# Kernel tuning notes

Hardware: AMD Instinct MI355X
Metric: run time of the kernel (lower is better)

The kernel has to match this reference:

```python
import jax, jax.numpy as jnp
import numpy as np


def setup_inputs() -> dict:
    key = jax.random.key(0)
    ks = jax.random.split(key, 6)
    B, C_in, C_out, H, W = 4, 256, 128, 64, 64
    return {
        "p": jax.random.normal(ks[0], (B, C_in, H, W), dtype=jnp.float32),
        "b": jax.random.normal(ks[1], (B, C_in, H, W), dtype=jnp.float32),
        "Wq": jax.random.normal(ks[2], (C_out, C_in), dtype=jnp.float32) * 0.05,
        "bq": jax.random.normal(ks[3], (C_out,), dtype=jnp.float32) * 0.05,
        "Wk": jax.random.normal(ks[4], (C_out, C_in), dtype=jnp.float32) * 0.05,
        "bk": jax.random.normal(ks[5], (C_out,), dtype=jnp.float32) * 0.05,
    }


def reference(p, b, Wq, bq, Wk, bk):
    # p, b: [B, C, H, W]; 1x1 convs are per-pixel GEMMs over channels.
    B, C, H, W = p.shape
    N = H * W
    p_flat = p.reshape(B, C, N)  # [B, C, N]
    b_flat = b.reshape(B, C, N)  # [B, C, N]
    # query = Conv1x1(p) -> [B, O, N] -> permuted to [B, N, O]
    q = jnp.einsum("bcn,oc->bno", p_flat, Wq) + bq  # [B, N, O]
    # key = Conv1x1(b) -> [B, O, N]
    k = jnp.einsum("bcn,oc->bon", b_flat, Wk) + bk[:, None]  # [B, O, N]
    energy = jnp.einsum("bno,bom->bnm", q, k)  # [B, N, N]
    attention = jax.nn.softmax(energy, axis=-1)
    # value = b flattened, attention applied over spatial tokens
    out = jnp.einsum("bnm,bcm->bcn", attention, b_flat)  # [B, C, N]
    return out.reshape(B, C, H, W)
```

## Files before the change

### kernel.cpp

```cpp
#include <hip/hip_runtime.h>
#include <stdint.h>


#define B_ 4
#define C_ 256
#define O_ 128
#define N_ 4096

#define AP 72
#define PP 40

typedef float v4f __attribute__((ext_vector_type(4)));
typedef short v8s __attribute__((ext_vector_type(8)));
typedef _Float16 v8h __attribute__((ext_vector_type(8)));
typedef uint32_t u32;
typedef unsigned short u16;

__device__ __forceinline__ u16 bf16_rne(float f) {
  u32 u = __builtin_bit_cast(u32, f);
  u += 0x7fffu + ((u >> 16) & 1u);
  return (u16)(u >> 16);
}
__device__ __forceinline__ float bf16_f(u16 s) {
  u32 u = ((u32)s) << 16;
  return __builtin_bit_cast(float, u);
}
__device__ __forceinline__ u16 f16_rne(float f) {
  _Float16 h = (_Float16)f;
  return __builtin_bit_cast(u16, h);
}
__device__ __forceinline__ float f16_f(u16 s) {
  return (float)__builtin_bit_cast(_Float16, s);
}
__device__ __forceinline__ v4f mfma16(v8s a, v8s b, v4f c) {
  return __builtin_amdgcn_mfma_f32_16x16x32_bf16(a, b, c, 0, 0, 0);
}
__device__ __forceinline__ v4f mfma16h(v8h a, v8h b, v4f c) {
  return __builtin_amdgcn_mfma_f32_16x16x32_f16(a, b, c, 0, 0, 0);
}
__device__ __forceinline__ void gl16(const u16* g, u16* l) {
  __builtin_amdgcn_global_load_lds(
      (const __attribute__((address_space(1))) u32*)g,
      (__attribute__((address_space(3))) u32*)l, 16, 0, 0);
}
template <int CTRL>
__device__ __forceinline__ float dppadd(float x) {
  int yi = __builtin_amdgcn_update_dpp(0, __builtin_bit_cast(int, x), CTRL,
                                       0xf, 0xf, true);
  return x + __builtin_bit_cast(float, yi);
}
__device__ __forceinline__ float sum16(float x) {
  x = dppadd<0xB1>(x);
  x = dppadd<0x4E>(x);
  x = dppadd<0x141>(x);
  x = dppadd<0x140>(x);
  return x;
}

__global__ __launch_bounds__(256) void k_proj(
    const float* __restrict__ Xp, const float* __restrict__ Wq,
    const float* __restrict__ bq, const float* __restrict__ Xb,
    const float* __restrict__ Wk, const float* __restrict__ bk,
    u16* __restrict__ Qh, u16* __restrict__ Ql, u16* __restrict__ Kh,
    u16* __restrict__ Vbf) {
  __shared__ __align__(16) short ah[64 * AP];
  __shared__ __align__(16) short al[64 * AP];
  __shared__ __align__(16) short wh[128 * AP];
  __shared__ __align__(16) short wl[128 * AP];
  const int tid = threadIdx.x;
  const int inst = blockIdx.x >> 8;
  const float* X = inst ? Xb : Xp;
  const float* W = inst ? Wk : Wq;
  const float* bias = inst ? bk : bq;
  const int b = (blockIdx.x >> 6) & 3;
  const int n0 = (blockIdx.x & 63) << 6;
  const int w = tid >> 6, lane = tid & 63, l15 = lane & 15, quad = lane >> 4;
  v4f acc[8];
#pragma unroll
  for (int t = 0; t < 8; t++) acc[t] = (v4f){0.f, 0.f, 0.f, 0.f};

  for (int c0 = 0; c0 < C_; c0 += 64) {
    __syncthreads();
    {
      const int c = tid >> 2, nch = (tid & 3) << 4;
      const float* s = X + ((size_t)(b * C_ + c0 + c)) * N_ + n0 + nch;
      float4 f0 = ((const float4*)s)[0], f1 = ((const float4*)s)[1],
             f2 = ((const float4*)s)[2], f3 = ((const float4*)s)[3];
      float v[16] = {f0.x, f0.y, f0.z, f0.w, f1.x, f1.y, f1.z, f1.w,
                     f2.x, f2.y, f2.z, f2.w, f3.x, f3.y, f3.z, f3.w};
      u16 hh[16];
#pragma unroll
      for (int j = 0; j < 16; j++) {
        u16 h = bf16_rne(v[j]);
        u16 l = bf16_rne(v[j] - bf16_f(h));
        hh[j] = h;
        ah[(nch + j) * AP + c] = (short)h;
        al[(nch + j) * AP + c] = (short)l;
      }
      if (inst) {
        u32 pk[8];
#pragma unroll
        for (int jj = 0; jj < 8; jj++)
          pk[jj] = (u32)hh[2 * jj] | ((u32)hh[2 * jj + 1] << 16);
        u16* vd = Vbf + ((size_t)(b * C_ + c0 + c)) * N_ + n0 + nch;
        ((uint4*)vd)[0] = make_uint4(pk[0], pk[1], pk[2], pk[3]);
        ((uint4*)vd)[1] = make_uint4(pk[4], pk[5], pk[6], pk[7]);
      }
    }
    {
      const int o = tid >> 1, cch = (tid & 1) << 5;
      const float* s = W + (size_t)o * C_ + c0 + cch;
#pragma unroll
      for (int jj = 0; jj < 8; jj++) {
        float4 f = ((const float4*)s)[jj];
        float v[4] = {f.x, f.y, f.z, f.w};
#pragma unroll
        for (int j = 0; j < 4; j++) {
          u16 h = bf16_rne(v[j]);
          u16 l = bf16_rne(v[j] - bf16_f(h));
          wh[o * AP + cch + jj * 4 + j] = (short)h;
          wl[o * AP + cch + jj * 4 + j] = (short)l;
        }
      }
    }
    __syncthreads();
#pragma unroll
    for (int s = 0; s < 2; s++) {
      v8s a_h = *(const v8s*)&ah[(16 * w + l15) * AP + 32 * s + 8 * quad];
      v8s a_l = *(const v8s*)&al[(16 * w + l15) * AP + 32 * s + 8 * quad];
#pragma unroll
      for (int to = 0; to < 8; to++) {
        v8s b_h = *(const v8s*)&wh[(16 * to + l15) * AP + 32 * s + 8 * quad];
        v8s b_l = *(const v8s*)&wl[(16 * to + l15) * AP + 32 * s + 8 * quad];
        acc[to] = mfma16(a_h, b_h, acc[to]);
        acc[to] = mfma16(a_h, b_l, acc[to]);
        acc[to] = mfma16(a_l, b_h, acc[to]);
      }
    }
  }
#pragma unroll
  for (int to = 0; to < 8; to++) {
    const int o = 16 * to + l15;
    const float bv = bias[o];
#pragma unroll
    for (int r = 0; r < 4; r++) {
      const int n = n0 + 16 * w + 4 * quad + r;
      float v = acc[to][r] + bv;
      const size_t idx = (size_t)(b * N_ + n) * O_ + o;
      if (!inst) {
        u16 h = f16_rne(v);
        Qh[idx] = h;
        Ql[idx] = f16_rne(v - f16_f(h));
      } else {
        Kh[idx] = f16_rne(v);
      }
    }
  }
}

__global__ __launch_bounds__(256, 2) void k_flash(
    const u16* __restrict__ Qh, const u16* __restrict__ Ql,
    const u16* __restrict__ Khp, const u16* __restrict__ Vbf,
    u16* __restrict__ Opart, float* __restrict__ lpart) {
  __shared__ __align__(16) short smem[27136];
  short* Pt = smem + 24576;

  const int tid = threadIdx.x;
  const int w = tid >> 6, lane = tid & 63, l15 = lane & 15, quad = lane >> 4;
  const int h = blockIdx.x & 1;
  const int qt = (blockIdx.x >> 1) & 63;
  const int b = blockIdx.x >> 7;
  const int n0 = qt << 6;
  const int tok0 = h << 11;

  const u16* khb = Khp + (size_t)b * N_ * O_;
  const u16* vb = Vbf + (size_t)b * C_ * N_;

  v8h qh[4], ql[4];
  {
    const u16* qrh = Qh + (size_t)(b * N_ + n0 + 16 * w + l15) * O_;
    const u16* qrl = Ql + (size_t)(b * N_ + n0 + 16 * w + l15) * O_;
#pragma unroll
    for (int s = 0; s < 4; s++) {
      qh[s] = *(const v8h*)(qrh + 32 * s + 8 * quad);
      ql[s] = *(const v8h*)(qrl + 32 * s + 8 * quad);
    }
  }

  v4f oacc[16];
#pragma unroll
  for (int t = 0; t < 16; t++) oacc[t] = (v4f){0.f, 0.f, 0.f, 0.f};
  float lstate[4] = {0.f, 0.f, 0.f, 0.f};

  auto stage = [&](int mtn, int bi) {
    const int m0n = tok0 + (mtn << 5);
    short* kd = smem + bi * 12288;
    short* vd = kd + 4096;
#pragma unroll
    for (int i = 0; i < 2; i++) {
      const int R = 8 * w + 4 * i;
      const int rl = R + (lane >> 4);
      const int cg = (lane & 15) ^ (rl & 15);
      gl16(khb + ((size_t)(m0n + rl) << 7) + (cg << 3), (u16*)(kd + (R << 7)));
    }
#pragma unroll
    for (int i = 0; i < 4; i++) {
      const int R = 64 * w + 16 * i;
      const int rl = R + (lane >> 2);
      const int cg = (lane & 3) ^ ((rl >> 1) & 3);
      gl16(vb + (size_t)rl * N_ + m0n + (cg << 3), (u16*)(vd + (R << 5)));
    }
  };

  stage(0, 0);

#pragma unroll 1
  for (int mt = 0; mt < 64; mt++) {
    const int pr = mt & 1;
    __syncthreads();
    if (mt + 1 < 64) stage(mt + 1, 1 - pr);
    const short* kc = smem + pr * 12288;
    const short* vc = kc + 4096;

    v4f eh[2], el[2];
#pragma unroll
    for (int t = 0; t < 2; t++) {
      eh[t] = (v4f){0.f, 0.f, 0.f, 0.f};
      el[t] = (v4f){0.f, 0.f, 0.f, 0.f};
    }
#pragma unroll
    for (int s = 0; s < 4; s++) {
#pragma unroll
      for (int t = 0; t < 2; t++) {
        const int off = ((16 * t + l15) << 7) + (((4 * s + quad) ^ l15) << 3);
        const v8h kf = *(const v8h*)&kc[off];
        eh[t] = mfma16h(qh[s], kf, eh[t]);
        el[t] = mfma16h(ql[s], kf, el[t]);
      }
    }

#pragma unroll
    for (int r = 0; r < 4; r++) {
      float p0 = __expf(eh[0][r] + el[0][r]);
      float p1 = __expf(eh[1][r] + el[1][r]);
      lstate[r] += sum16(p0 + p1);
      Pt[(16 * w + 4 * quad + r) * PP + l15] = (short)bf16_rne(p0);
      Pt[(16 * w + 4 * quad + r) * PP + 16 + l15] = (short)bf16_rne(p1);
    }
    __builtin_amdgcn_s_waitcnt(0xC07F);
    asm volatile("s_barrier" ::: "memory");

    v8s af[4];
#pragma unroll
    for (int rw = 0; rw < 4; rw++)
      af[rw] = *(const v8s*)&Pt[(16 * rw + l15) * PP + 8 * quad];
#pragma unroll
    for (int cg = 0; cg < 4; cg++) {
      const int ch = 64 * w + 16 * cg + l15;
      const int voff = (ch << 5) + ((quad ^ ((ch >> 1) & 3)) << 3);
      const v8s vf = *(const v8s*)&vc[voff];
#pragma unroll
      for (int rw = 0; rw < 4; rw++)
        oacc[rw * 4 + cg] = mfma16(af[rw], vf, oacc[rw * 4 + cg]);
    }
  }

  __syncthreads();
  u16* outx = (u16*)smem;
#pragma unroll
  for (int rw = 0; rw < 4; rw++)
#pragma unroll
    for (int cg = 0; cg < 4; cg++) {
      const int ch = 64 * w + 16 * cg + l15;
      const v4f o = oacc[rw * 4 + cg];
      u32* q = (u32*)outx;
      const int base = ch * 36 + 8 * rw + 2 * quad;
      q[base] = (u32)bf16_rne(o[0]) | ((u32)bf16_rne(o[1]) << 16);
      q[base + 1] = (u32)bf16_rne(o[2]) | ((u32)bf16_rne(o[3]) << 16);
    }
  if (l15 == 0) {
#pragma unroll
    for (int r = 0; r < 4; r++)
      lpart[(size_t)blockIdx.x * 64 + 16 * w + 4 * quad + r] = lstate[r];
  }
  __syncthreads();
  {
    u16* od = Opart + (size_t)blockIdx.x * 16384;
    const int cr = tid >> 2, nch = (tid & 3) << 4;
#pragma unroll
    for (int it = 0; it < 4; it++) {
      const int c = cr + 64 * it;
      const u16* srcr = &outx[c * 72 + nch];
      uint4* dst = (uint4*)(od + c * 64 + nch);
      dst[0] = ((const uint4*)srcr)[0];
      dst[1] = ((const uint4*)srcr)[1];
    }
  }
}

__global__ __launch_bounds__(256) void k_merge(const u16* __restrict__ Opart,
                                               const float* __restrict__ lpart,
                                               float* __restrict__ out) {
  const int idx = blockIdx.x * 256 + threadIdx.x;
  const int e4 = idx << 2;
  const int b = e4 >> 20;
  const int c = (e4 >> 12) & 255;
  const int n = e4 & 4095;
  const int qt = n >> 6, row = n & 63;
  const int g = (b * 64 + qt) * 2;
  const u16* q0 = Opart + (size_t)g * 16384 + c * 64 + row;
  ushort4 a0 = *(const ushort4*)q0;
  ushort4 a1 = *(const ushort4*)(q0 + 16384);
  float4 l0 = *(const float4*)(lpart + (size_t)g * 64 + row);
  float4 l1 = *(const float4*)(lpart + (size_t)g * 64 + 64 + row);
  float4 o;
  o.x = (bf16_f(a0.x) + bf16_f(a1.x)) / (l0.x + l1.x);
  o.y = (bf16_f(a0.y) + bf16_f(a1.y)) / (l0.y + l1.y);
  o.z = (bf16_f(a0.z) + bf16_f(a1.z)) / (l0.z + l1.z);
  o.w = (bf16_f(a0.w) + bf16_f(a1.w)) / (l0.w + l1.w);
  *(float4*)(out + e4) = o;
}

extern "C" void kernel_launch(void* const* d_in, const int* in_sizes, int n_in,
                              void* d_out, int out_size, void* d_ws, size_t ws_size,
                              hipStream_t stream) {
  const float* p = (const float*)d_in[0];
  const float* bb = (const float*)d_in[1];
  const float* Wq = (const float*)d_in[2];
  const float* bq = (const float*)d_in[3];
  const float* Wk = (const float*)d_in[4];
  const float* bk = (const float*)d_in[5];
  float* out = (float*)d_out;

  const size_t plane = (size_t)B_ * N_ * O_;
  u16* Qh = (u16*)d_ws;
  u16* Ql = Qh + plane;
  u16* Kh = Ql + plane;
  u16* Vbf = Kh + plane;
  u16* Opart = Vbf + 2 * plane;
  float* lpart = (float*)(Opart + (size_t)512 * 16384);

  hipLaunchKernelGGL(k_proj, dim3(512), dim3(256), 0, stream, p, Wq, bq, bb,
                     Wk, bk, Qh, Ql, Kh, Vbf);
  hipLaunchKernelGGL(k_flash, dim3(B_ * 64 * 2), dim3(256), 0, stream, Qh, Ql,
                     Kh, Vbf, Opart, lpart);
  hipLaunchKernelGGL(k_merge, dim3((B_ * C_ * N_) / (256 * 4)), dim3(256), 0,
                     stream, Opart, lpart, out);
}
```

Baseline: 188.9 us.

## Split flash attention three ways and precompute bf16 weight splits

```diff
diff --git a/kernel.cpp b/kernel.cpp
--- a/kernel.cpp
+++ b/kernel.cpp
@@ -57,20 +57,53 @@
   return x;
 }
 
+__global__ __launch_bounds__(256) void k_wprep(const float* __restrict__ Wq,
+                                               const float* __restrict__ Wk,
+                                               u16* __restrict__ Wqh,
+                                               u16* __restrict__ Wql,
+                                               u16* __restrict__ Wkh,
+                                               u16* __restrict__ Wkl) {
+  const int inst = blockIdx.x >> 4;
+  const float* src = inst ? Wk : Wq;
+  u16* dh = inst ? Wkh : Wqh;
+  u16* dl = inst ? Wkl : Wql;
+  const int base = ((blockIdx.x & 15) * 256 + threadIdx.x) * 8;
+  float4 a = ((const float4*)(src + base))[0];
+  float4 c = ((const float4*)(src + base))[1];
+  float v[8] = {a.x, a.y, a.z, a.w, c.x, c.y, c.z, c.w};
+  u16 hh[8], ll[8];
+#pragma unroll
+  for (int j = 0; j < 8; j++) {
+    hh[j] = bf16_rne(v[j]);
+    ll[j] = bf16_rne(v[j] - bf16_f(hh[j]));
+  }
+  uint4 oh, ol;
+  oh.x = (u32)hh[0] | ((u32)hh[1] << 16);
+  oh.y = (u32)hh[2] | ((u32)hh[3] << 16);
+  oh.z = (u32)hh[4] | ((u32)hh[5] << 16);
+  oh.w = (u32)hh[6] | ((u32)hh[7] << 16);
+  ol.x = (u32)ll[0] | ((u32)ll[1] << 16);
+  ol.y = (u32)ll[2] | ((u32)ll[3] << 16);
+  ol.z = (u32)ll[4] | ((u32)ll[5] << 16);
+  ol.w = (u32)ll[6] | ((u32)ll[7] << 16);
+  *(uint4*)(dh + base) = oh;
+  *(uint4*)(dl + base) = ol;
+}
+
 __global__ __launch_bounds__(256) void k_proj(
-    const float* __restrict__ Xp, const float* __restrict__ Wq,
-    const float* __restrict__ bq, const float* __restrict__ Xb,
-    const float* __restrict__ Wk, const float* __restrict__ bk,
+    const float* __restrict__ Xp, const float* __restrict__ Xb,
+    const float* __restrict__ bq, const float* __restrict__ bk,
+    const u16* __restrict__ Wqh, const u16* __restrict__ Wql,
+    const u16* __restrict__ Wkh, const u16* __restrict__ Wkl,
     u16* __restrict__ Qh, u16* __restrict__ Ql, u16* __restrict__ Kh,
     u16* __restrict__ Vbf) {
   __shared__ __align__(16) short ah[64 * AP];
   __shared__ __align__(16) short al[64 * AP];
-  __shared__ __align__(16) short wh[128 * AP];
-  __shared__ __align__(16) short wl[128 * AP];
   const int tid = threadIdx.x;
   const int inst = blockIdx.x >> 8;
   const float* X = inst ? Xb : Xp;
-  const float* W = inst ? Wk : Wq;
+  const u16* Wh = inst ? Wkh : Wqh;
+  const u16* Wl = inst ? Wkl : Wql;
   const float* bias = inst ? bk : bq;
   const int b = (blockIdx.x >> 6) & 3;
   const int n0 = (blockIdx.x & 63) << 6;
@@ -79,59 +112,49 @@
 #pragma unroll
   for (int t = 0; t < 8; t++) acc[t] = (v4f){0.f, 0.f, 0.f, 0.f};
 
+  const int sn = tid & 63;
+  const int scg = tid >> 6;
+
   for (int c0 = 0; c0 < C_; c0 += 64) {
     __syncthreads();
     {
-      const int c = tid >> 2, nch = (tid & 3) << 4;
-      const float* s = X + ((size_t)(b * C_ + c0 + c)) * N_ + n0 + nch;
-      float4 f0 = ((const float4*)s)[0], f1 = ((const float4*)s)[1],
-             f2 = ((const float4*)s)[2], f3 = ((const float4*)s)[3];
-      float v[16] = {f0.x, f0.y, f0.z, f0.w, f1.x, f1.y, f1.z, f1.w,
-                     f2.x, f2.y, f2.z, f2.w, f3.x, f3.y, f3.z, f3.w};
-      u16 hh[16];
+      const float* s = X + ((size_t)(b * C_ + c0 + scg * 16)) * N_ + n0 + sn;
+      u16 hh[16], ll[16];
 #pragma unroll
       for (int j = 0; j < 16; j++) {
-        u16 h = bf16_rne(v[j]);
-        u16 l = bf16_rne(v[j] - bf16_f(h));
-        hh[j] = h;
-        ah[(nch + j) * AP + c] = (short)h;
-        al[(nch + j) * AP + c] = (short)l;
-      }
+        float v = s[(size_t)j * N_];
+        hh[j] = bf16_rne(v);
+        ll[j] = bf16_rne(v - bf16_f(hh[j]));
+      }
+      u32 ph[8], pl[8];
+#pragma unroll
+      for (int j = 0; j < 8; j++) {
+        ph[j] = (u32)hh[2 * j] | ((u32)hh[2 * j + 1] << 16);
+        pl[j] = (u32)ll[2 * j] | ((u32)ll[2 * j + 1] << 16);
+      }
+      uint4* dh = (uint4*)&ah[sn * AP + scg * 16];
+      uint4* dl = (uint4*)&al[sn * AP + scg * 16];
+      dh[0] = make_uint4(ph[0], ph[1], ph[2], ph[3]);
+      dh[1] = make_uint4(ph[4], ph[5], ph[6], ph[7]);
+      dl[0] = make_uint4(pl[0], pl[1], pl[2], pl[3]);
+      dl[1] = make_uint4(pl[4], pl[5], pl[6], pl[7]);
       if (inst) {
-        u32 pk[8];
-#pragma unroll
-        for (int jj = 0; jj < 8; jj++)
-          pk[jj] = (u32)hh[2 * jj] | ((u32)hh[2 * jj + 1] << 16);
-        u16* vd = Vbf + ((size_t)(b * C_ + c0 + c)) * N_ + n0 + nch;
-        ((uint4*)vd)[0] = make_uint4(pk[0], pk[1], pk[2], pk[3]);
-        ((uint4*)vd)[1] = make_uint4(pk[4], pk[5], pk[6], pk[7]);
-      }
-    }
-    {
-      const int o = tid >> 1, cch = (tid & 1) << 5;
-      const float* s = W + (size_t)o * C_ + c0 + cch;
-#pragma unroll
-      for (int jj = 0; jj < 8; jj++) {
-        float4 f = ((const float4*)s)[jj];
-        float v[4] = {f.x, f.y, f.z, f.w};
-#pragma unroll
-        for (int j = 0; j < 4; j++) {
-          u16 h = bf16_rne(v[j]);
-          u16 l = bf16_rne(v[j] - bf16_f(h));
-          wh[o * AP + cch + jj * 4 + j] = (short)h;
-          wl[o * AP + cch + jj * 4 + j] = (short)l;
-        }
+#pragma unroll
+        for (int j = 0; j < 16; j++)
+          Vbf[((size_t)(b * C_ + c0 + scg * 16 + j)) * N_ + n0 + sn] = hh[j];
       }
     }
     __syncthreads();
 #pragma unroll
-    for (int s = 0; s < 2; s++) {
-      v8s a_h = *(const v8s*)&ah[(16 * w + l15) * AP + 32 * s + 8 * quad];
-      v8s a_l = *(const v8s*)&al[(16 * w + l15) * AP + 32 * s + 8 * quad];
+    for (int s2 = 0; s2 < 2; s2++) {
+      v8s a_h = *(const v8s*)&ah[(16 * w + l15) * AP + 32 * s2 + 8 * quad];
+      v8s a_l = *(const v8s*)&al[(16 * w + l15) * AP + 32 * s2 + 8 * quad];
 #pragma unroll
       for (int to = 0; to < 8; to++) {
-        v8s b_h = *(const v8s*)&wh[(16 * to + l15) * AP + 32 * s + 8 * quad];
-        v8s b_l = *(const v8s*)&wl[(16 * to + l15) * AP + 32 * s + 8 * quad];
+        const u16* wp = Wh + (size_t)(16 * to + l15) * C_ + c0 + 32 * s2 + 8 * quad;
+        const u16* wp2 = Wl + (size_t)(16 * to + l15) * C_ + c0 + 32 * s2 + 8 * quad;
+        v8s b_h = *(const v8s*)wp;
+        v8s b_l = *(const v8s*)wp2;
         acc[to] = mfma16(a_h, b_h, acc[to]);
         acc[to] = mfma16(a_h, b_l, acc[to]);
         acc[to] = mfma16(a_l, b_h, acc[to]);
@@ -158,7 +181,7 @@
   }
 }
 
-__global__ __launch_bounds__(256, 2) void k_flash(
+__global__ __launch_bounds__(256, 3) void k_flash(
     const u16* __restrict__ Qh, const u16* __restrict__ Ql,
     const u16* __restrict__ Khp, const u16* __restrict__ Vbf,
     u16* __restrict__ Opart, float* __restrict__ lpart) {
@@ -167,11 +190,13 @@
 
   const int tid = threadIdx.x;
   const int w = tid >> 6, lane = tid & 63, l15 = lane & 15, quad = lane >> 4;
-  const int h = blockIdx.x & 1;
-  const int qt = (blockIdx.x >> 1) & 63;
-  const int b = blockIdx.x >> 7;
+  const int bq = blockIdx.x / 3;
+  const int h = blockIdx.x - bq * 3;
+  const int qt = bq & 63;
+  const int b = bq >> 6;
   const int n0 = qt << 6;
-  const int tok0 = h << 11;
+  const int tok0 = h * 1344;
+  const int niter = (h == 2) ? 44 : 42;
 
   const u16* khb = Khp + (size_t)b * N_ * O_;
   const u16* vb = Vbf + (size_t)b * C_ * N_;
@@ -215,10 +240,10 @@
   stage(0, 0);
 
 #pragma unroll 1
-  for (int mt = 0; mt < 64; mt++) {
+  for (int mt = 0; mt < niter; mt++) {
     const int pr = mt & 1;
     __syncthreads();
-    if (mt + 1 < 64) stage(mt + 1, 1 - pr);
+    if (mt + 1 < niter) stage(mt + 1, 1 - pr);
     const short* kc = smem + pr * 12288;
     const short* vc = kc + 4096;
 
@@ -307,17 +332,19 @@
   const int c = (e4 >> 12) & 255;
   const int n = e4 & 4095;
   const int qt = n >> 6, row = n & 63;
-  const int g = (b * 64 + qt) * 2;
+  const int g = (b * 64 + qt) * 3;
   const u16* q0 = Opart + (size_t)g * 16384 + c * 64 + row;
   ushort4 a0 = *(const ushort4*)q0;
   ushort4 a1 = *(const ushort4*)(q0 + 16384);
+  ushort4 a2 = *(const ushort4*)(q0 + 32768);
   float4 l0 = *(const float4*)(lpart + (size_t)g * 64 + row);
   float4 l1 = *(const float4*)(lpart + (size_t)g * 64 + 64 + row);
+  float4 l2 = *(const float4*)(lpart + (size_t)g * 64 + 128 + row);
   float4 o;
-  o.x = (bf16_f(a0.x) + bf16_f(a1.x)) / (l0.x + l1.x);
-  o.y = (bf16_f(a0.y) + bf16_f(a1.y)) / (l0.y + l1.y);
-  o.z = (bf16_f(a0.z) + bf16_f(a1.z)) / (l0.z + l1.z);
-  o.w = (bf16_f(a0.w) + bf16_f(a1.w)) / (l0.w + l1.w);
+  o.x = (bf16_f(a0.x) + bf16_f(a1.x) + bf16_f(a2.x)) / (l0.x + l1.x + l2.x);
+  o.y = (bf16_f(a0.y) + bf16_f(a1.y) + bf16_f(a2.y)) / (l0.y + l1.y + l2.y);
+  o.z = (bf16_f(a0.z) + bf16_f(a1.z) + bf16_f(a2.z)) / (l0.z + l1.z + l2.z);
+  o.w = (bf16_f(a0.w) + bf16_f(a1.w) + bf16_f(a2.w)) / (l0.w + l1.w + l2.w);
   *(float4*)(out + e4) = o;
 }
 
@@ -337,12 +364,18 @@
   u16* Ql = Qh + plane;
   u16* Kh = Ql + plane;
   u16* Vbf = Kh + plane;
-  u16* Opart = Vbf + 2 * plane;
-  float* lpart = (float*)(Opart + (size_t)512 * 16384);
-
-  hipLaunchKernelGGL(k_proj, dim3(512), dim3(256), 0, stream, p, Wq, bq, bb,
-                     Wk, bk, Qh, Ql, Kh, Vbf);
-  hipLaunchKernelGGL(k_flash, dim3(B_ * 64 * 2), dim3(256), 0, stream, Qh, Ql,
+  u16* Wqh = Vbf + 2 * plane;
+  u16* Wql = Wqh + 32768;
+  u16* Wkh = Wql + 32768;
+  u16* Wkl = Wkh + 32768;
+  u16* Opart = Wkl + 32768;
+  float* lpart = (float*)(Opart + (size_t)768 * 16384);
+
+  hipLaunchKernelGGL(k_wprep, dim3(32), dim3(256), 0, stream, Wq, Wk, Wqh, Wql,
+                     Wkh, Wkl);
+  hipLaunchKernelGGL(k_proj, dim3(512), dim3(256), 0, stream, p, bb, bq, bk,
+                     Wqh, Wql, Wkh, Wkl, Qh, Ql, Kh, Vbf);
+  hipLaunchKernelGGL(k_flash, dim3(B_ * 64 * 3), dim3(256), 0, stream, Qh, Ql,
                      Kh, Vbf, Opart, lpart);
   hipLaunchKernelGGL(k_merge, dim3((B_ * C_ * N_) / (256 * 4)), dim3(256), 0,
                      stream, Opart, lpart, out);
```

Result: slower. 225.5 us (+19.4%).
